# Optimization experiments

Hardware: AMD Instinct MI355X
Metric: run time of the kernel (lower is better)

## Reference

```python
import jax, jax.numpy as jnp
import numpy as np

N = 50000        # nodes
E = 800000       # edges (avg degree 16)
D_IN = 128
D_OUT = 128
P_DROP = 0.1
BN_EPS = 1e-5


def setup_inputs() -> dict:
    key = jax.random.key(0)
    k1, k2, k3 = jax.random.split(key, 3)
    x = jax.random.normal(k1, (N, D_IN), dtype=jnp.float32)
    edge_index = jax.random.randint(k2, (2, E), 0, N, dtype=jnp.int64)
    W = jax.random.normal(k3, (D_IN, D_OUT), dtype=jnp.float32) / np.sqrt(D_IN).astype(np.float32)
    b = jnp.zeros((D_OUT,), jnp.float32)
    bn_gamma = jnp.ones((D_OUT,), jnp.float32)
    bn_beta = jnp.zeros((D_OUT,), jnp.float32)
    return {"x": x, "edge_index": edge_index, "W": W, "b": b,
            "bn_gamma": bn_gamma, "bn_beta": bn_beta}


def reference(x, edge_index, W, b, bn_gamma, bn_beta):
    n = x.shape[0]
    # --- GCNConv: h = x W, symmetric-normalized aggregation with self-loops ---
    h = x @ W                                            # [N, D_OUT]
    loops = jnp.arange(n, dtype=edge_index.dtype)
    src = jnp.concatenate([edge_index[0], loops])        # [E+N]
    dst = jnp.concatenate([edge_index[1], loops])        # [E+N]
    deg = jax.ops.segment_sum(jnp.ones_like(dst, h.dtype), dst, num_segments=n)
    dinv = jax.lax.rsqrt(jnp.maximum(deg, 1.0))          # deg >= 1 (self-loops)
    norm = dinv[src] * dinv[dst]                         # [E+N]
    msg = h[src] * norm[:, None]                         # gather + weight
    z = jax.ops.segment_sum(msg, dst, num_segments=n) + b
    # --- activation ---
    z = jax.nn.relu(z)
    # --- BatchNorm over nodes (training-mode batch statistics) ---
    mean = z.mean(axis=0)
    var = z.var(axis=0)
    z = bn_gamma * (z - mean) * jax.lax.rsqrt(var + BN_EPS) + bn_beta
    # --- dropout (training mode, fixed key for determinism) ---
    keep = jax.random.bernoulli(jax.random.key(42), 1.0 - P_DROP, z.shape)
    z = jnp.where(keep, z / (1.0 - P_DROP), 0.0)
    return z.astype(x.dtype)
```

## Files before the change

### kernel.cpp

```cpp
#include <hip/hip_runtime.h>
#include <stdint.h>


#define NN 50000
#define NE 800000
#define DD 128
#define SCAN_B 256
#define NSB ((NN + SCAN_B - 1) / SCAN_B)

__device__ __forceinline__ uint32_t rotl32(uint32_t x, uint32_t d) {
  return (x << d) | (x >> (32u - d));
}

__device__ __forceinline__ uint32_t threefry_bits(uint32_t idx) {
  const uint32_t ks0 = 0u;
  const uint32_t ks1 = 42u;
  const uint32_t ks2 = 0x1BD11BDAu ^ ks0 ^ ks1;
  uint32_t x0 = ks0;
  uint32_t x1 = idx + ks1;
#define TF_R(r) { x0 += x1; x1 = rotl32(x1, (r)); x1 ^= x0; }
  TF_R(13u) TF_R(15u) TF_R(26u) TF_R(6u)
  x0 += ks1; x1 += ks2 + 1u;
  TF_R(17u) TF_R(29u) TF_R(16u) TF_R(24u)
  x0 += ks2; x1 += ks0 + 2u;
  TF_R(13u) TF_R(15u) TF_R(26u) TF_R(6u)
  x0 += ks0; x1 += ks1 + 3u;
  TF_R(17u) TF_R(29u) TF_R(16u) TF_R(24u)
  x0 += ks1; x1 += ks2 + 4u;
  TF_R(13u) TF_R(15u) TF_R(26u) TF_R(6u)
  x0 += ks2; x1 += ks0 + 5u;
#undef TF_R
  return x0 ^ x1;
}

__device__ __forceinline__ uint32_t f2bf(float f) {
  uint32_t u = __float_as_uint(f);
  return (u + 0x7fffu + ((u >> 16) & 1u)) >> 16;
}
__device__ __forceinline__ float bf_lo(uint32_t p) { return __uint_as_float(p << 16); }
__device__ __forceinline__ float bf_hi(uint32_t p) { return __uint_as_float(p & 0xffff0000u); }

#define BM 128
#define BK 32
__global__ __launch_bounds__(256) void k_gemm(const float* __restrict__ x,
                                              const float* __restrict__ Wm,
                                              uint16_t* __restrict__ hbf) {
  __shared__ float xs[BM][BK + 1];
  __shared__ float wsh[BK][DD];
  const int t = threadIdx.x;
  const int row0 = blockIdx.x * BM;
  const int tx = t & 15, ty = t >> 4;
  const int c0 = tx * 8, r0 = ty * 8;
  float acc[8][8] = {};

  for (int kc = 0; kc < DD; kc += BK) {
#pragma unroll
    for (int q = 0; q < 4; ++q) {
      int s = t + q * 256;
      int r = s >> 3;
      int kq = s & 7;
      int grow = row0 + r;
      float4 v = make_float4(0.f, 0.f, 0.f, 0.f);
      if (grow < NN)
        v = *reinterpret_cast<const float4*>(&x[(size_t)grow * DD + kc + kq * 4]);
      xs[r][kq * 4 + 0] = v.x;
      xs[r][kq * 4 + 1] = v.y;
      xs[r][kq * 4 + 2] = v.z;
      xs[r][kq * 4 + 3] = v.w;
    }
#pragma unroll
    for (int q = 0; q < 4; ++q) {
      int s = t + q * 256;
      int kr = s >> 5;
      int cq = s & 31;
      float4 v = *reinterpret_cast<const float4*>(&Wm[(size_t)(kc + kr) * DD + cq * 4]);
      *reinterpret_cast<float4*>(&wsh[kr][cq * 4]) = v;
    }
    __syncthreads();
#pragma unroll
    for (int kk = 0; kk < BK; ++kk) {
      float a[8];
#pragma unroll
      for (int i = 0; i < 8; ++i) a[i] = xs[r0 + i][kk];
      float4 wv0 = *reinterpret_cast<const float4*>(&wsh[kk][c0]);
      float4 wv1 = *reinterpret_cast<const float4*>(&wsh[kk][c0 + 4]);
      float w[8] = {wv0.x, wv0.y, wv0.z, wv0.w, wv1.x, wv1.y, wv1.z, wv1.w};
#pragma unroll
      for (int i = 0; i < 8; ++i)
#pragma unroll
        for (int j = 0; j < 8; ++j)
          acc[i][j] = fmaf(a[i], w[j], acc[i][j]);
    }
    __syncthreads();
  }
#pragma unroll
  for (int i = 0; i < 8; ++i) {
    int grow = row0 + r0 + i;
    if (grow < NN) {
      uint32_t p0 = f2bf(acc[i][0]) | (f2bf(acc[i][1]) << 16);
      uint32_t p1 = f2bf(acc[i][2]) | (f2bf(acc[i][3]) << 16);
      uint32_t p2 = f2bf(acc[i][4]) | (f2bf(acc[i][5]) << 16);
      uint32_t p3 = f2bf(acc[i][6]) | (f2bf(acc[i][7]) << 16);
      *reinterpret_cast<uint4*>(&hbf[(size_t)grow * DD + c0]) = make_uint4(p0, p1, p2, p3);
    }
  }
}

__global__ void k_count(const int* __restrict__ ei, int* __restrict__ cnt,
                        int* __restrict__ pos) {
  int e = blockIdx.x * blockDim.x + threadIdx.x;
  if (e < NE) pos[e] = atomicAdd(&cnt[ei[NE + e]], 1);
}

__global__ __launch_bounds__(SCAN_B) void k_scan1(const int* __restrict__ cnt,
                                                  int* __restrict__ tmp,
                                                  int* __restrict__ blk_sums) {
  __shared__ int sm[SCAN_B];
  int t = threadIdx.x;
  int i = blockIdx.x * SCAN_B + t;
  int v = (i < NN) ? cnt[i] : 0;
  sm[t] = v;
  __syncthreads();
  for (int off = 1; off < SCAN_B; off <<= 1) {
    int u = (t >= off) ? sm[t - off] : 0;
    __syncthreads();
    sm[t] += u;
    __syncthreads();
  }
  if (i < NN) tmp[i] = sm[t];
  if (t == SCAN_B - 1) blk_sums[blockIdx.x] = sm[t];
}

__global__ __launch_bounds__(SCAN_B) void k_scan2(const int* __restrict__ blk_sums,
                                                  int* __restrict__ blk_off) {
  __shared__ int sm[SCAN_B];
  int t = threadIdx.x;
  int v = (t < NSB) ? blk_sums[t] : 0;
  sm[t] = v;
  __syncthreads();
  for (int off = 1; off < SCAN_B; off <<= 1) {
    int u = (t >= off) ? sm[t - off] : 0;
    __syncthreads();
    sm[t] += u;
    __syncthreads();
  }
  if (t < NSB) blk_off[t] = sm[t] - v;
}

__global__ void k_scan3(const int* __restrict__ tmp, const int* __restrict__ blk_off,
                        const int* __restrict__ cnt, int* __restrict__ row_ptr,
                        float* __restrict__ dinv) {
  int i = blockIdx.x * SCAN_B + threadIdx.x;
  if (i < NN) {
    row_ptr[i + 1] = tmp[i] + blk_off[i >> 8];
    if (i == 0) row_ptr[0] = 0;
    dinv[i] = rsqrtf((float)cnt[i] + 1.0f);
  }
}

__global__ void k_fill(const int* __restrict__ ei, const int* __restrict__ row_ptr,
                       const int* __restrict__ pos, int* __restrict__ colv) {
  int e = blockIdx.x * blockDim.x + threadIdx.x;
  if (e < NE) {
    int d = ei[NE + e];
    colv[row_ptr[d] + pos[e]] = ei[e];
  }
}

__global__ __launch_bounds__(256) void k_agg(const uint16_t* __restrict__ hbf,
                                             const int* __restrict__ row_ptr,
                                             const int* __restrict__ colv,
                                             const float* __restrict__ dinv,
                                             const float* __restrict__ bias,
                                             float* __restrict__ z) {
  int wave = threadIdx.x >> 6;
  int lane = threadIdx.x & 63;
  int node = blockIdx.x * 4 + wave;
  if (node >= NN) return;
  const uint32_t* hp = reinterpret_cast<const uint32_t*>(hbf);

  float di = dinv[node];
  float w0 = di * di;
  uint32_t ms = hp[(size_t)node * 64 + lane];
  float ax = bf_lo(ms) * w0, ay = bf_hi(ms) * w0;

  int e = row_ptr[node], end = row_ptr[node + 1];
  while (e + 8 <= end) {
    int s[8]; float w[8]; uint32_t m[8];
#pragma unroll
    for (int q = 0; q < 8; ++q) s[q] = colv[e + q];
#pragma unroll
    for (int q = 0; q < 8; ++q) { w[q] = dinv[s[q]]; m[q] = hp[(size_t)s[q] * 64 + lane]; }
#pragma unroll
    for (int q = 0; q < 8; ++q) {
      float wq = w[q] * di;
      ax = fmaf(bf_lo(m[q]), wq, ax);
      ay = fmaf(bf_hi(m[q]), wq, ay);
    }
    e += 8;
  }
  while (e < end) {
    int s0 = colv[e];
    float wq = dinv[s0] * di;
    uint32_t m0 = hp[(size_t)s0 * 64 + lane];
    ax = fmaf(bf_lo(m0), wq, ax);
    ay = fmaf(bf_hi(m0), wq, ay);
    ++e;
  }
  float2 bb = reinterpret_cast<const float2*>(bias)[lane];
  float zx = fmaxf(ax + bb.x, 0.f);
  float zy = fmaxf(ay + bb.y, 0.f);
  reinterpret_cast<float2*>(z)[(size_t)node * 64 + lane] = make_float2(zx, zy);
}

__global__ __launch_bounds__(256) void k_stats(const float* __restrict__ z,
                                               float* __restrict__ bn_sum,
                                               float* __restrict__ bn_sumsq) {
  int t = threadIdx.x;
  int c = t & 127;
  int half = t >> 7;
  float s = 0.f, s2 = 0.f;
  for (int r = blockIdx.x * 2 + half; r < NN; r += gridDim.x * 2) {
    float v = z[(size_t)r * DD + c];
    s += v;
    s2 = fmaf(v, v, s2);
  }
  __shared__ float sm[256], sm2[256];
  sm[t] = s; sm2[t] = s2;
  __syncthreads();
  if (t < 128) {
    atomicAdd(&bn_sum[c], sm[t] + sm[t + 128]);
    atomicAdd(&bn_sumsq[c], sm2[t] + sm2[t + 128]);
  }
}

__global__ __launch_bounds__(256) void k_final(float* __restrict__ z,
                                               const float* __restrict__ bn_sum,
                                               const float* __restrict__ bn_sumsq,
                                               const float* __restrict__ gamma,
                                               const float* __restrict__ beta) {
  int j = blockIdx.x * blockDim.x + threadIdx.x;
  if (j >= NN * DD) return;
  int c = j & 127;
  const float invN = 1.0f / (float)NN;
  float mean = bn_sum[c] * invN;
  float var = bn_sumsq[c] * invN - mean * mean;
  float rs = rsqrtf(var + 1e-5f);
  float val = (z[j] - mean) * rs * gamma[c] + beta[c];
  uint32_t bits = threefry_bits((uint32_t)j);
  float u = __uint_as_float((bits >> 9) | 0x3f800000u) - 1.0f;
  z[j] = (u < 0.9f) ? val * (1.0f / 0.9f) : 0.0f;
}

extern "C" void kernel_launch(void* const* d_in, const int* in_sizes, int n_in,
                              void* d_out, int out_size, void* d_ws, size_t ws_size,
                              hipStream_t stream) {
  const float* x     = (const float*)d_in[0];
  const int*   ei    = (const int*)d_in[1];
  const float* Wm    = (const float*)d_in[2];
  const float* bvec  = (const float*)d_in[3];
  const float* gamma = (const float*)d_in[4];
  const float* beta  = (const float*)d_in[5];
  float* zout = (float*)d_out;

  uint16_t* hbf  = (uint16_t*)d_ws;
  int* colv      = (int*)(hbf + (size_t)NN * DD);
  int* pos       = colv + NE;
  int* cnt       = pos + NE;
  float* bn_sum  = (float*)(cnt + NN);
  float* bn_sumsq= bn_sum + DD;
  int* tmp_scan  = (int*)(bn_sumsq + DD);
  int* row_ptr   = tmp_scan + NN;
  float* dinv    = (float*)(row_ptr + NN + 1);
  int* blk_sums  = (int*)(dinv + NN);
  int* blk_off   = blk_sums + NSB;

  hipMemsetAsync(cnt, 0, (size_t)(NN + 2 * DD) * sizeof(int), stream);

  k_gemm<<<(NN + BM - 1) / BM, 256, 0, stream>>>(x, Wm, hbf);
  k_count<<<(NE + 255) / 256, 256, 0, stream>>>(ei, cnt, pos);
  k_scan1<<<NSB, SCAN_B, 0, stream>>>(cnt, tmp_scan, blk_sums);
  k_scan2<<<1, SCAN_B, 0, stream>>>(blk_sums, blk_off);
  k_scan3<<<NSB, SCAN_B, 0, stream>>>(tmp_scan, blk_off, cnt, row_ptr, dinv);
  k_fill<<<(NE + 255) / 256, 256, 0, stream>>>(ei, row_ptr, pos, colv);
  k_agg<<<(NN + 3) / 4, 256, 0, stream>>>(hbf, row_ptr, colv, dinv, bvec, zout);
  k_stats<<<400, 256, 0, stream>>>(zout, bn_sum, bn_sumsq);
  k_final<<<(NN * DD + 255) / 256, 256, 0, stream>>>(zout, bn_sum, bn_sumsq, gamma, beta);
}
```

Before: 180.2 us.

## Use split-bf16 MFMA GEMM, pipeline aggregation loads, vectorize stats and final

```diff
diff --git a/kernel.cpp b/kernel.cpp
--- a/kernel.cpp
+++ b/kernel.cpp
@@ -7,6 +7,9 @@
 #define DD 128
 #define SCAN_B 256
 #define NSB ((NN + SCAN_B - 1) / SCAN_B)
+
+using f32x4  = __attribute__((ext_vector_type(4))) float;
+using short8 = __attribute__((ext_vector_type(8))) short;
 
 __device__ __forceinline__ uint32_t rotl32(uint32_t x, uint32_t d) {
   return (x << d) | (x >> (32u - d));
@@ -37,71 +40,106 @@
   uint32_t u = __float_as_uint(f);
   return (u + 0x7fffu + ((u >> 16) & 1u)) >> 16;
 }
+__device__ __forceinline__ float bf2f(uint32_t h) { return __uint_as_float(h << 16); }
 __device__ __forceinline__ float bf_lo(uint32_t p) { return __uint_as_float(p << 16); }
 __device__ __forceinline__ float bf_hi(uint32_t p) { return __uint_as_float(p & 0xffff0000u); }
 
-#define BM 128
-#define BK 32
+__global__ __launch_bounds__(256) void k_wpack(const float* __restrict__ Wm,
+                                               short8* __restrict__ wfh,
+                                               short8* __restrict__ wfl) {
+  int tid = blockIdx.x * 256 + threadIdx.x;
+  if (tid >= 32 * 64) return;
+  int lane = tid & 63;
+  int cfks = tid >> 6;
+  int ks = cfks >> 3, cf = cfks & 7;
+  int krow = ks * 32 + ((lane >> 4) << 3);
+  int col = cf * 16 + (lane & 15);
+  short8 h, l;
+#pragma unroll
+  for (int j = 0; j < 8; ++j) {
+    float w = Wm[(size_t)(krow + j) * DD + col];
+    uint32_t hb = f2bf(w);
+    uint32_t lb = f2bf(w - bf2f(hb));
+    h[j] = (short)hb;
+    l[j] = (short)lb;
+  }
+  wfh[tid] = h;
+  wfl[tid] = l;
+}
+
+#define GBM 128
 __global__ __launch_bounds__(256) void k_gemm(const float* __restrict__ x,
-                                              const float* __restrict__ Wm,
+                                              const short8* __restrict__ wfh,
+                                              const short8* __restrict__ wfl,
                                               uint16_t* __restrict__ hbf) {
-  __shared__ float xs[BM][BK + 1];
-  __shared__ float wsh[BK][DD];
+  __shared__ uint4 ldsbuf[4096];
+  char* lds = (char*)ldsbuf;
   const int t = threadIdx.x;
-  const int row0 = blockIdx.x * BM;
-  const int tx = t & 15, ty = t >> 4;
-  const int c0 = tx * 8, r0 = ty * 8;
-  float acc[8][8] = {};
-
-  for (int kc = 0; kc < DD; kc += BK) {
-#pragma unroll
-    for (int q = 0; q < 4; ++q) {
-      int s = t + q * 256;
-      int r = s >> 3;
-      int kq = s & 7;
-      int grow = row0 + r;
-      float4 v = make_float4(0.f, 0.f, 0.f, 0.f);
-      if (grow < NN)
-        v = *reinterpret_cast<const float4*>(&x[(size_t)grow * DD + kc + kq * 4]);
-      xs[r][kq * 4 + 0] = v.x;
-      xs[r][kq * 4 + 1] = v.y;
-      xs[r][kq * 4 + 2] = v.z;
-      xs[r][kq * 4 + 3] = v.w;
-    }
-#pragma unroll
-    for (int q = 0; q < 4; ++q) {
-      int s = t + q * 256;
-      int kr = s >> 5;
-      int cq = s & 31;
-      float4 v = *reinterpret_cast<const float4*>(&Wm[(size_t)(kc + kr) * DD + cq * 4]);
-      *reinterpret_cast<float4*>(&wsh[kr][cq * 4]) = v;
-    }
-    __syncthreads();
-#pragma unroll
-    for (int kk = 0; kk < BK; ++kk) {
-      float a[8];
-#pragma unroll
-      for (int i = 0; i < 8; ++i) a[i] = xs[r0 + i][kk];
-      float4 wv0 = *reinterpret_cast<const float4*>(&wsh[kk][c0]);
-      float4 wv1 = *reinterpret_cast<const float4*>(&wsh[kk][c0 + 4]);
-      float w[8] = {wv0.x, wv0.y, wv0.z, wv0.w, wv1.x, wv1.y, wv1.z, wv1.w};
-#pragma unroll
-      for (int i = 0; i < 8; ++i)
-#pragma unroll
-        for (int j = 0; j < 8; ++j)
-          acc[i][j] = fmaf(a[i], w[j], acc[i][j]);
-    }
-    __syncthreads();
-  }
-#pragma unroll
-  for (int i = 0; i < 8; ++i) {
-    int grow = row0 + r0 + i;
+  const int row0 = blockIdx.x * GBM;
+  const int c4 = t & 31, rbase = t >> 5;
+
+#pragma unroll
+  for (int i = 0; i < 16; ++i) {
+    int r = rbase + i * 8;
+    int grow = row0 + r;
+    float4 v = make_float4(0.f, 0.f, 0.f, 0.f);
+    if (grow < NN)
+      v = *reinterpret_cast<const float4*>(&x[(size_t)grow * DD + c4 * 4]);
+    uint32_t h0 = f2bf(v.x), h1 = f2bf(v.y), h2 = f2bf(v.z), h3 = f2bf(v.w);
+    uint32_t l0 = f2bf(v.x - bf2f(h0)), l1 = f2bf(v.y - bf2f(h1));
+    uint32_t l2 = f2bf(v.z - bf2f(h2)), l3 = f2bf(v.w - bf2f(h3));
+    int byte = (r * 256 + c4 * 8) ^ ((r & 7) << 4);
+    *reinterpret_cast<uint2*>(lds + byte) = make_uint2(h0 | (h1 << 16), h2 | (h3 << 16));
+    *reinterpret_cast<uint2*>(lds + 32768 + byte) = make_uint2(l0 | (l1 << 16), l2 | (l3 << 16));
+  }
+  __syncthreads();
+
+  const int wv = t >> 6, l = t & 63;
+  f32x4 acc[2][8] = {};
+#pragma unroll
+  for (int ks = 0; ks < 4; ++ks) {
+    short8 ah[2], al[2];
+#pragma unroll
+    for (int rf = 0; rf < 2; ++rf) {
+      int r = wv * 32 + rf * 16 + (l & 15);
+      int byte = (r * 256 + ks * 64 + ((l >> 4) << 4)) ^ ((r & 7) << 4);
+      ah[rf] = *reinterpret_cast<const short8*>(lds + byte);
+      al[rf] = *reinterpret_cast<const short8*>(lds + 32768 + byte);
+    }
+#pragma unroll
+    for (int cf = 0; cf < 8; ++cf) {
+      short8 bh = wfh[(ks * 8 + cf) * 64 + l];
+      short8 bl = wfl[(ks * 8 + cf) * 64 + l];
+#pragma unroll
+      for (int rf = 0; rf < 2; ++rf) {
+        acc[rf][cf] = __builtin_amdgcn_mfma_f32_16x16x32_bf16(ah[rf], bl, acc[rf][cf], 0, 0, 0);
+        acc[rf][cf] = __builtin_amdgcn_mfma_f32_16x16x32_bf16(al[rf], bh, acc[rf][cf], 0, 0, 0);
+        acc[rf][cf] = __builtin_amdgcn_mfma_f32_16x16x32_bf16(ah[rf], bh, acc[rf][cf], 0, 0, 0);
+      }
+    }
+  }
+  __syncthreads();
+
+#pragma unroll
+  for (int rf = 0; rf < 2; ++rf)
+#pragma unroll
+    for (int cf = 0; cf < 8; ++cf)
+#pragma unroll
+      for (int i = 0; i < 4; ++i) {
+        int row = wv * 32 + rf * 16 + ((l >> 4) << 2) + i;
+        int col = cf * 16 + (l & 15);
+        int byte = (row * 256 + col * 2) ^ ((row & 7) << 4);
+        *reinterpret_cast<uint16_t*>(lds + byte) = (uint16_t)f2bf(acc[rf][cf][i]);
+      }
+  __syncthreads();
+#pragma unroll
+  for (int i = 0; i < 16; ++i) {
+    int r = rbase + i * 8;
+    int grow = row0 + r;
     if (grow < NN) {
-      uint32_t p0 = f2bf(acc[i][0]) | (f2bf(acc[i][1]) << 16);
-      uint32_t p1 = f2bf(acc[i][2]) | (f2bf(acc[i][3]) << 16);
-      uint32_t p2 = f2bf(acc[i][4]) | (f2bf(acc[i][5]) << 16);
-      uint32_t p3 = f2bf(acc[i][6]) | (f2bf(acc[i][7]) << 16);
-      *reinterpret_cast<uint4*>(&hbf[(size_t)grow * DD + c0]) = make_uint4(p0, p1, p2, p3);
+      int byte = (r * 256 + c4 * 8) ^ ((r & 7) << 4);
+      uint2 v = *reinterpret_cast<const uint2*>(lds + byte);
+      *reinterpret_cast<uint2*>(&hbf[(size_t)grow * DD + c4 * 4]) = v;
     }
   }
 }
@@ -184,29 +222,45 @@
   uint32_t ms = hp[(size_t)node * 64 + lane];
   float ax = bf_lo(ms) * w0, ay = bf_hi(ms) * w0;
 
-  int e = row_ptr[node], end = row_ptr[node + 1];
-  while (e + 8 <= end) {
-    int s[8]; float w[8]; uint32_t m[8];
-#pragma unroll
-    for (int q = 0; q < 8; ++q) s[q] = colv[e + q];
-#pragma unroll
-    for (int q = 0; q < 8; ++q) { w[q] = dinv[s[q]]; m[q] = hp[(size_t)s[q] * 64 + lane]; }
-#pragma unroll
-    for (int q = 0; q < 8; ++q) {
-      float wq = w[q] * di;
-      ax = fmaf(bf_lo(m[q]), wq, ax);
-      ay = fmaf(bf_hi(m[q]), wq, ay);
-    }
-    e += 8;
-  }
-  while (e < end) {
-    int s0 = colv[e];
-    float wq = dinv[s0] * di;
-    uint32_t m0 = hp[(size_t)s0 * 64 + lane];
-    ax = fmaf(bf_lo(m0), wq, ax);
-    ay = fmaf(bf_hi(m0), wq, ay);
-    ++e;
-  }
+  int beg = row_ptr[node], end = row_ptr[node + 1];
+
+  float wA[8], wB[8];
+  uint32_t mA[8], mB[8];
+
+#define AGG_LOAD(W, M, e0)                                        \
+  do {                                                            \
+    _Pragma("unroll")                                             \
+    for (int q = 0; q < 8; ++q) {                                 \
+      int ee = (e0) + q;                                          \
+      bool ok = ee < end;                                         \
+      int idx = ok ? ee : 0;                                      \
+      int ss = colv[idx];                                         \
+      W[q] = ok ? dinv[ss] * di : 0.f;                            \
+      M[q] = hp[(size_t)ss * 64 + lane];                          \
+    }                                                             \
+  } while (0)
+
+#define AGG_FMA(W, M)                                             \
+  do {                                                            \
+    _Pragma("unroll")                                             \
+    for (int q = 0; q < 8; ++q) {                                 \
+      ax = fmaf(bf_lo(M[q]), W[q], ax);                           \
+      ay = fmaf(bf_hi(M[q]), W[q], ay);                           \
+    }                                                             \
+  } while (0)
+
+  if (beg < end) {
+    int nbat = (end - beg + 7) >> 3;
+    AGG_LOAD(wA, mA, beg);
+    for (int b = 1; b < nbat; ++b) {
+      if (b & 1) { AGG_LOAD(wB, mB, beg + b * 8); AGG_FMA(wA, mA); }
+      else       { AGG_LOAD(wA, mA, beg + b * 8); AGG_FMA(wB, mB); }
+    }
+    if (nbat & 1) AGG_FMA(wA, mA); else AGG_FMA(wB, mB);
+  }
+#undef AGG_LOAD
+#undef AGG_FMA
+
   float2 bb = reinterpret_cast<const float2*>(bias)[lane];
   float zx = fmaxf(ax + bb.x, 0.f);
   float zy = fmaxf(ay + bb.y, 0.f);
@@ -217,20 +271,32 @@
                                                float* __restrict__ bn_sum,
                                                float* __restrict__ bn_sumsq) {
   int t = threadIdx.x;
-  int c = t & 127;
-  int half = t >> 7;
-  float s = 0.f, s2 = 0.f;
-  for (int r = blockIdx.x * 2 + half; r < NN; r += gridDim.x * 2) {
-    float v = z[(size_t)r * DD + c];
-    s += v;
-    s2 = fmaf(v, v, s2);
-  }
-  __shared__ float sm[256], sm2[256];
-  sm[t] = s; sm2[t] = s2;
-  __syncthreads();
-  if (t < 128) {
-    atomicAdd(&bn_sum[c], sm[t] + sm[t + 128]);
-    atomicAdd(&bn_sumsq[c], sm2[t] + sm2[t + 128]);
+  int c4 = t & 31;
+  int rgrp = t >> 5;
+  float sx = 0.f, sy = 0.f, sz = 0.f, sw = 0.f;
+  float qx = 0.f, qy = 0.f, qz = 0.f, qw = 0.f;
+  for (int r = blockIdx.x * 8 + rgrp; r < NN; r += gridDim.x * 8) {
+    float4 v = *reinterpret_cast<const float4*>(&z[(size_t)r * DD + c4 * 4]);
+    sx += v.x; sy += v.y; sz += v.z; sw += v.w;
+    qx = fmaf(v.x, v.x, qx); qy = fmaf(v.y, v.y, qy);
+    qz = fmaf(v.z, v.z, qz); qw = fmaf(v.w, v.w, qw);
+  }
+  __shared__ float4 sm[256], sm2[256];
+  sm[t] = make_float4(sx, sy, sz, sw);
+  sm2[t] = make_float4(qx, qy, qz, qw);
+  __syncthreads();
+  if (t < 32) {
+    float4 a = sm[t], b = sm2[t];
+#pragma unroll
+    for (int g = 1; g < 8; ++g) {
+      float4 u = sm[t + 32 * g], v = sm2[t + 32 * g];
+      a.x += u.x; a.y += u.y; a.z += u.z; a.w += u.w;
+      b.x += v.x; b.y += v.y; b.z += v.z; b.w += v.w;
+    }
+    atomicAdd(&bn_sum[t * 4 + 0], a.x); atomicAdd(&bn_sum[t * 4 + 1], a.y);
+    atomicAdd(&bn_sum[t * 4 + 2], a.z); atomicAdd(&bn_sum[t * 4 + 3], a.w);
+    atomicAdd(&bn_sumsq[t * 4 + 0], b.x); atomicAdd(&bn_sumsq[t * 4 + 1], b.y);
+    atomicAdd(&bn_sumsq[t * 4 + 2], b.z); atomicAdd(&bn_sumsq[t * 4 + 3], b.w);
   }
 }
 
@@ -239,17 +305,31 @@
                                                const float* __restrict__ bn_sumsq,
                                                const float* __restrict__ gamma,
                                                const float* __restrict__ beta) {
-  int j = blockIdx.x * blockDim.x + threadIdx.x;
-  if (j >= NN * DD) return;
-  int c = j & 127;
+  int j4 = blockIdx.x * blockDim.x + threadIdx.x;
+  if (j4 >= NN * DD / 4) return;
+  int c4 = j4 & 31;
   const float invN = 1.0f / (float)NN;
-  float mean = bn_sum[c] * invN;
-  float var = bn_sumsq[c] * invN - mean * mean;
-  float rs = rsqrtf(var + 1e-5f);
-  float val = (z[j] - mean) * rs * gamma[c] + beta[c];
-  uint32_t bits = threefry_bits((uint32_t)j);
-  float u = __uint_as_float((bits >> 9) | 0x3f800000u) - 1.0f;
-  z[j] = (u < 0.9f) ? val * (1.0f / 0.9f) : 0.0f;
+  float4 s = *reinterpret_cast<const float4*>(&bn_sum[c4 * 4]);
+  float4 q = *reinterpret_cast<const float4*>(&bn_sumsq[c4 * 4]);
+  float4 g = *reinterpret_cast<const float4*>(&gamma[c4 * 4]);
+  float4 bt = *reinterpret_cast<const float4*>(&beta[c4 * 4]);
+  float4 v = *reinterpret_cast<const float4*>(&z[(size_t)j4 * 4]);
+  float out[4];
+  float mm[4] = {s.x * invN, s.y * invN, s.z * invN, s.w * invN};
+  float qq[4] = {q.x * invN, q.y * invN, q.z * invN, q.w * invN};
+  float gg[4] = {g.x, g.y, g.z, g.w};
+  float bb[4] = {bt.x, bt.y, bt.z, bt.w};
+  float vv[4] = {v.x, v.y, v.z, v.w};
+#pragma unroll
+  for (int i = 0; i < 4; ++i) {
+    float var = qq[i] - mm[i] * mm[i];
+    float rs = rsqrtf(var + 1e-5f);
+    float val = (vv[i] - mm[i]) * rs * gg[i] + bb[i];
+    uint32_t bits = threefry_bits((uint32_t)(j4 * 4 + i));
+    float u = __uint_as_float((bits >> 9) | 0x3f800000u) - 1.0f;
+    out[i] = (u < 0.9f) ? val * (1.0f / 0.9f) : 0.0f;
+  }
+  *reinterpret_cast<float4*>(&z[(size_t)j4 * 4]) = make_float4(out[0], out[1], out[2], out[3]);
 }
 
 extern "C" void kernel_launch(void* const* d_in, const int* in_sizes, int n_in,
@@ -264,7 +344,9 @@
   float* zout = (float*)d_out;
 
   uint16_t* hbf  = (uint16_t*)d_ws;
-  int* colv      = (int*)(hbf + (size_t)NN * DD);
+  short8* wfh    = (short8*)(hbf + (size_t)NN * DD);
+  short8* wfl    = wfh + 2048;
+  int* colv      = (int*)(wfl + 2048);
   int* pos       = colv + NE;
   int* cnt       = pos + NE;
   float* bn_sum  = (float*)(cnt + NN);
@@ -277,7 +359,8 @@
 
   hipMemsetAsync(cnt, 0, (size_t)(NN + 2 * DD) * sizeof(int), stream);
 
-  k_gemm<<<(NN + BM - 1) / BM, 256, 0, stream>>>(x, Wm, hbf);
+  k_wpack<<<8, 256, 0, stream>>>(Wm, wfh, wfl);
+  k_gemm<<<(NN + GBM - 1) / GBM, 256, 0, stream>>>(x, wfh, wfl, hbf);
   k_count<<<(NE + 255) / 256, 256, 0, stream>>>(ei, cnt, pos);
   k_scan1<<<NSB, SCAN_B, 0, stream>>>(cnt, tmp_scan, blk_sums);
   k_scan2<<<1, SCAN_B, 0, stream>>>(blk_sums, blk_off);
@@ -285,5 +368,5 @@
   k_fill<<<(NE + 255) / 256, 256, 0, stream>>>(ei, row_ptr, pos, colv);
   k_agg<<<(NN + 3) / 4, 256, 0, stream>>>(hbf, row_ptr, colv, dinv, bvec, zout);
   k_stats<<<400, 256, 0, stream>>>(zout, bn_sum, bn_sumsq);
-  k_final<<<(NN * DD + 255) / 256, 256, 0, stream>>>(zout, bn_sum, bn_sumsq, gamma, beta);
-}
+  k_final<<<(NN * DD / 4 + 255) / 256, 256, 0, stream>>>(zout, bn_sum, bn_sumsq, gamma, beta);
+}
```

After: 243.3 us. +35.0%, slower.
